# Performance work log

Hardware: AMD Instinct MI355X
Metric: run time of the kernel (lower is better)

Reference implementation:

```python
import jax, jax.numpy as jnp
import numpy as np

B, D_IN, R, D_P, K, D_C, ITERS = 4096, 2048, 7, 128, 25, 16, 3


def _ln(x, g, b, eps=1e-5):
    m = jnp.mean(x, axis=-1, keepdims=True)
    v = jnp.var(x, axis=-1, keepdims=True)
    return (x - m) * jax.lax.rsqrt(v + eps) * g + b


def _squash(x):
    eps = 1e-6
    ns = jnp.sum(x * x, axis=-1, keepdims=True)
    scale = ns / jnp.maximum(1.0 + ns, eps)
    return scale * x / (jnp.sqrt(ns) + eps)


def setup_inputs() -> dict:
    key = jax.random.key(0)
    ks = jax.random.split(key, 8)
    f = lambda k, shp, s=0.02: (jax.random.normal(k, shp) * s).astype(jnp.float32)
    return {
        "z": jax.random.normal(ks[0], (B, D_IN), jnp.float32),
        "W_prim": f(ks[1], (D_IN, R * D_P)),
        "b_prim": jnp.zeros((R * D_P,), jnp.float32),
        "ln_a_g": jnp.ones((D_IN,), jnp.float32),
        "ln_a_b": jnp.zeros((D_IN,), jnp.float32),
        "W_act": f(ks[2], (D_IN, R)),
        "b_act": jnp.zeros((R,), jnp.float32),
        "w_caps": (np.sqrt(K / (D_P * R)).astype(np.float32)
                   * jax.random.normal(ks[3], (R, D_P, K, D_C))).astype(jnp.float32),
        "ln_c_g": jnp.ones((D_C,), jnp.float32),
        "ln_c_b": jnp.zeros((D_C,), jnp.float32),
        "beta_u": f(ks[4], (K,), 1.0),
        "ln_h_g": jnp.ones((R * D_C,), jnp.float32),
        "ln_h_b": jnp.zeros((R * D_C,), jnp.float32),
        "W_h1": f(ks[5], (R * D_C, 4 * R * D_C)),
        "b_h1": jnp.zeros((4 * R * D_C,), jnp.float32),
        "W_h2": f(ks[6], (4 * R * D_C, 1)),
        "b_h2": jnp.zeros((1,), jnp.float32),
    }


def reference(z, W_prim, b_prim, ln_a_g, ln_a_b, W_act, b_act, w_caps,
              ln_c_g, ln_c_b, beta_u, ln_h_g, ln_h_b, W_h1, b_h1, W_h2, b_h2):
    # primary capsules: [B, R, D_P] poses + [B, R] activations
    pose = _squash((z @ W_prim + b_prim).reshape(B, R, D_P))
    act = jnp.clip(jax.nn.sigmoid(_ln(z, ln_a_g, ln_a_b) @ W_act + b_act), 0.0, 1.0)

    # votes: [B, R, K, D_C]
    u = jnp.einsum('brd,rdkh->brkh', pose, w_caps)
    scale = 1.0 / np.sqrt(D_C).astype(np.float32)

    # iterative routing (EM/softmax-agreement style)
    q = jnp.full((B, R, K), 1.0 / K, dtype=z.dtype)
    class_pose = None
    for _ in range(ITERS):
        wts = q * act[:, :, None]                               # [B,R,K]
        class_pose = _ln(jnp.einsum('brk,brkh->bkh', wts, u), ln_c_g, ln_c_b)
        agree = jnp.einsum('bkh,brkh->brk', class_pose, u) * scale
        q = jax.nn.softmax(agree, axis=-1)

    class_act = jax.nn.sigmoid(beta_u[None, :] + jnp.einsum('brk,br->bk', q, act))
    route_class_emb = q[..., None] * u                          # [B,R,K,D_C]

    # concat per-route interaction vectors -> [B, K, R*D_C]
    class_embed = jnp.transpose(route_class_emb, (0, 2, 1, 3)).reshape(B, K, R * D_C)
    h = jax.nn.gelu(_ln(class_embed, ln_h_g, ln_h_b) @ W_h1 + b_h1, approximate=False)
    logits = (h @ W_h2 + b_h2)[..., 0]                          # [B, K]

    return (logits, class_embed, class_pose, class_act, q, pose, act, route_class_emb)
```

## Files before the change

### kernel.cpp

```cpp
#include <hip/hip_runtime.h>
#include <cstddef>

#define BB 4096
#define DIN 2048
#define RR 7
#define DP 128
#define KK 25
#define DC 16
#define NITERS 3
#define RKH (RR*KK*DC)
#define RK  (RR*KK)
#define KH  (KK*DC)
#define HD  (RR*DC)
#define H4  (4*HD)

typedef __attribute__((ext_vector_type(8))) short bf16x8;
typedef __attribute__((ext_vector_type(4))) float f32x4;

__device__ __forceinline__ unsigned pk_bf16(float a, float b) {
    union { float f; unsigned u; } xa, xb;
    xa.f = a; xb.f = b;
    unsigned ua = (xa.u + 0x7FFFu + ((xa.u >> 16) & 1u)) >> 16;
    unsigned ub = (xb.u + 0x7FFFu + ((xb.u >> 16) & 1u)) >> 16;
    return (ua & 0xFFFFu) | (ub << 16);
}

__device__ __forceinline__ float gelu_tanh(float x) {
    float x3 = x * x * x;
    float tt = 0.7978845608f * (x + 0.044715f * x3);
    float e = __expf(2.0f * tt);
    float th = 1.0f - 2.0f / (e + 1.0f);
    return 0.5f * x * (1.0f + th);
}

__global__ __launch_bounds__(256) void transpose_cvt_kernel(
    const float* __restrict__ src, unsigned short* __restrict__ dst, int RS, int CS)
{
    __shared__ float T[64][65];
    int r0 = blockIdx.x * 64, c0 = blockIdx.y * 64;
    size_t bo = (size_t)blockIdx.z * RS * CS;
    src += bo; dst += bo;
    int t = threadIdx.x;
    for (int s = t; s < 64 * 16; s += 256) {
        int row = s >> 4, c4 = s & 15;
        int gr = r0 + row, gc = c0 + c4 * 4;
        float4 v = make_float4(0.f, 0.f, 0.f, 0.f);
        if (gr < RS && gc < CS) v = *(const float4*)(src + (size_t)gr * CS + gc);
        T[row][c4 * 4 + 0] = v.x; T[row][c4 * 4 + 1] = v.y;
        T[row][c4 * 4 + 2] = v.z; T[row][c4 * 4 + 3] = v.w;
    }
    __syncthreads();
    for (int s = t; s < 64 * 16; s += 256) {
        int col = s >> 4, r4 = s & 15;
        int gc = c0 + col, gr = r0 + r4 * 4;
        if (gc < CS && gr + 3 < RS) {
            unsigned lo = pk_bf16(T[r4 * 4 + 0][col], T[r4 * 4 + 1][col]);
            unsigned hi = pk_bf16(T[r4 * 4 + 2][col], T[r4 * 4 + 3][col]);
            *(uint2*)(dst + (size_t)gc * RS + gr) = make_uint2(lo, hi);
        }
    }
}

__global__ __launch_bounds__(256) void act_kernel(
    const float* __restrict__ z, const float* __restrict__ g, const float* __restrict__ bb,
    const float* __restrict__ Wa, const float* __restrict__ ba,
    float* __restrict__ act_out)
{
    int b = blockIdx.x;
    int t = threadIdx.x;
    __shared__ float zs[DIN];
    __shared__ float ws1[4], ws2[4];
    __shared__ float wr[4][RR];
    const float* zr = z + (size_t)b * DIN;
    float s = 0.f, s2 = 0.f;
    for (int i = t; i < DIN; i += 256) {
        float v = zr[i]; zs[i] = v; s += v; s2 += v * v;
    }
    for (int off = 32; off; off >>= 1) { s += __shfl_down(s, off); s2 += __shfl_down(s2, off); }
    int w = t >> 6, lane = t & 63;
    if (lane == 0) { ws1[w] = s; ws2[w] = s2; }
    __syncthreads();
    s  = ws1[0] + ws1[1] + ws1[2] + ws1[3];
    s2 = ws2[0] + ws2[1] + ws2[2] + ws2[3];
    float mean = s * (1.0f / DIN);
    float var  = s2 * (1.0f / DIN) - mean * mean;
    float rstd = rsqrtf(var + 1e-5f);
    float acc[RR];
#pragma unroll
    for (int r = 0; r < RR; ++r) acc[r] = 0.f;
    for (int i = t; i < DIN; i += 256) {
        float y = (zs[i] - mean) * rstd * g[i] + bb[i];
#pragma unroll
        for (int r = 0; r < RR; ++r) acc[r] += y * Wa[i * RR + r];
    }
    for (int off = 32; off; off >>= 1) {
#pragma unroll
        for (int r = 0; r < RR; ++r) acc[r] += __shfl_down(acc[r], off);
    }
    if (lane == 0) {
#pragma unroll
        for (int r = 0; r < RR; ++r) wr[w][r] = acc[r];
    }
    __syncthreads();
    if (t < RR) {
        float v = wr[0][t] + wr[1][t] + wr[2][t] + wr[3][t] + ba[t];
        float sg = 1.0f / (1.0f + expf(-v));
        sg = fminf(fmaxf(sg, 0.0f), 1.0f);
        act_out[(size_t)b * RR + t] = sg;
    }
}

__global__ __launch_bounds__(256) void pose_mfma(
    const float* __restrict__ z, const unsigned short* __restrict__ WpT,
    const float* __restrict__ bp, float* __restrict__ pose_out)
{
    __shared__ __align__(16) unsigned short As[128 * 40];
    __shared__ __align__(16) unsigned short Bs[128 * 40];
    __shared__ float sq[2][128];
    int m0 = blockIdx.x * 128, r = blockIdx.y, t = threadIdx.x;
    int n0 = r * DP;
    int w = t >> 6, l = t & 63;
    int lrow = l & 15, koff = l >> 4;
    int rbase = (w >> 1) * 64, cbase = (w & 1) * 64;
    f32x4 acc[4][4];
#pragma unroll
    for (int i = 0; i < 4; ++i)
#pragma unroll
        for (int j = 0; j < 4; ++j) acc[i][j] = 0.0f;
    for (int kt = 0; kt < DIN; kt += 32) {
#pragma unroll
        for (int q = 0; q < 4; ++q) {
            int s = t + 256 * q;
            int row = s >> 3, k4 = s & 7;
            float4 v = *(const float4*)(z + (size_t)(m0 + row) * DIN + kt + k4 * 4);
            *(uint2*)(As + row * 40 + k4 * 4) = make_uint2(pk_bf16(v.x, v.y), pk_bf16(v.z, v.w));
        }
#pragma unroll
        for (int q = 0; q < 2; ++q) {
            int s = t + 256 * q;
            int col = s >> 2, k8 = s & 3;
            uint4 v = *(const uint4*)(WpT + (size_t)(n0 + col) * DIN + kt + k8 * 8);
            *(uint4*)(Bs + col * 40 + k8 * 8) = v;
        }
        __syncthreads();
        bf16x8 a[4], b[4];
#pragma unroll
        for (int i = 0; i < 4; ++i)
            a[i] = *(const bf16x8*)(As + (rbase + i * 16 + lrow) * 40 + koff * 8);
#pragma unroll
        for (int j = 0; j < 4; ++j)
            b[j] = *(const bf16x8*)(Bs + (cbase + j * 16 + lrow) * 40 + koff * 8);
#pragma unroll
        for (int i = 0; i < 4; ++i)
#pragma unroll
            for (int j = 0; j < 4; ++j)
                acc[i][j] = __builtin_amdgcn_mfma_f32_16x16x32_bf16(a[i], b[j], acc[i][j], 0, 0, 0);
        __syncthreads();
    }
    float bpv[4];
#pragma unroll
    for (int j = 0; j < 4; ++j) bpv[j] = bp[n0 + cbase + j * 16 + lrow];
    float ns_[4][4];
#pragma unroll
    for (int i = 0; i < 4; ++i)
#pragma unroll
        for (int reg = 0; reg < 4; ++reg) {
            float ss = 0.f;
#pragma unroll
            for (int j = 0; j < 4; ++j) {
                float x = acc[i][j][reg] + bpv[j];
                acc[i][j][reg] = x;
                ss += x * x;
            }
            ss += __shfl_xor(ss, 1); ss += __shfl_xor(ss, 2);
            ss += __shfl_xor(ss, 4); ss += __shfl_xor(ss, 8);
            ns_[i][reg] = ss;
        }
    if (lrow == 0) {
#pragma unroll
        for (int i = 0; i < 4; ++i)
#pragma unroll
            for (int reg = 0; reg < 4; ++reg)
                sq[w & 1][rbase + i * 16 + koff * 4 + reg] = ns_[i][reg];
    }
    __syncthreads();
#pragma unroll
    for (int i = 0; i < 4; ++i)
#pragma unroll
        for (int reg = 0; reg < 4; ++reg) {
            int rl = rbase + i * 16 + koff * 4 + reg;
            float ns = sq[0][rl] + sq[1][rl];
            float factor = (ns / fmaxf(1.0f + ns, 1e-6f)) / (sqrtf(ns) + 1e-6f);
            size_t rowbase = ((size_t)(m0 + rl) * RR + r) * DP;
#pragma unroll
            for (int j = 0; j < 4; ++j)
                pose_out[rowbase + cbase + j * 16 + lrow] = acc[i][j][reg] * factor;
        }
}

__global__ __launch_bounds__(256) void votes_mfma(
    const float* __restrict__ pose, const unsigned short* __restrict__ wcT,
    float* __restrict__ u_out)
{
    __shared__ __align__(16) unsigned short As[128 * 152];
    __shared__ __align__(16) unsigned short Bs[80 * 152];
    int m0 = blockIdx.x * 128, r = blockIdx.y, n0 = blockIdx.z * 80;
    int t = threadIdx.x;
    int w = t >> 6, l = t & 63;
    int lrow = l & 15, koff = l >> 4;
    int rbase = w * 32;
#pragma unroll
    for (int q = 0; q < 16; ++q) {
        int s = t + 256 * q;
        int row = s >> 5, k4 = s & 31;
        float4 v = *(const float4*)(pose + ((size_t)(m0 + row) * RR + r) * DP + k4 * 4);
        *(uint2*)(As + row * 152 + k4 * 4) = make_uint2(pk_bf16(v.x, v.y), pk_bf16(v.z, v.w));
    }
    const unsigned short* wr_ = wcT + (size_t)r * KH * DP;
#pragma unroll
    for (int q = 0; q < 5; ++q) {
        int s = t + 256 * q;
        int col = s >> 4, k8 = s & 15;
        uint4 v = *(const uint4*)(wr_ + (size_t)(n0 + col) * DP + k8 * 8);
        *(uint4*)(Bs + col * 152 + k8 * 8) = v;
    }
    __syncthreads();
    f32x4 acc[2][5];
#pragma unroll
    for (int i = 0; i < 2; ++i)
#pragma unroll
        for (int j = 0; j < 5; ++j) acc[i][j] = 0.0f;
#pragma unroll
    for (int ks = 0; ks < 4; ++ks) {
        bf16x8 a[2], b[5];
#pragma unroll
        for (int i = 0; i < 2; ++i)
            a[i] = *(const bf16x8*)(As + (rbase + i * 16 + lrow) * 152 + ks * 32 + koff * 8);
#pragma unroll
        for (int j = 0; j < 5; ++j)
            b[j] = *(const bf16x8*)(Bs + (j * 16 + lrow) * 152 + ks * 32 + koff * 8);
#pragma unroll
        for (int i = 0; i < 2; ++i)
#pragma unroll
            for (int j = 0; j < 5; ++j)
                acc[i][j] = __builtin_amdgcn_mfma_f32_16x16x32_bf16(a[i], b[j], acc[i][j], 0, 0, 0);
    }
#pragma unroll
    for (int i = 0; i < 2; ++i)
#pragma unroll
        for (int reg = 0; reg < 4; ++reg) {
            int row = m0 + rbase + i * 16 + koff * 4 + reg;
            size_t base = ((size_t)row * RR + r) * KH + n0;
#pragma unroll
            for (int j = 0; j < 5; ++j)
                u_out[base + j * 16 + lrow] = acc[i][j][reg];
        }
}

__global__ __launch_bounds__(64) void routing_kernel(
    const float* __restrict__ u_in, const float* __restrict__ act_in,
    const float* __restrict__ lncg, const float* __restrict__ lncb,
    const float* __restrict__ beta_u,
    float* __restrict__ q_out, float* __restrict__ cp_out,
    float* __restrict__ ca_out, float* __restrict__ rce_out,
    float* __restrict__ ce_out)
{
    __shared__ __align__(16) float U[RKH];
    __shared__ float Q[RK];
    __shared__ float CP[KH];
    __shared__ float AG[RK];
    __shared__ float A7[RR];
    int b = blockIdx.x, t = threadIdx.x;
    const float4* u4 = (const float4*)(u_in + (size_t)b * RKH);
    float4* U4 = (float4*)U;
    for (int p = t; p < RKH / 4; p += 64) U4[p] = u4[p];
    if (t < RR) A7[t] = act_in[(size_t)b * RR + t];
    for (int p = t; p < RK; p += 64) Q[p] = 1.0f / KK;
    __syncthreads();
    for (int it = 0; it < NITERS; ++it) {
        for (int p = t; p < KH; p += 64) {
            int k = p / DC;
            float s = 0.f;
#pragma unroll
            for (int r = 0; r < RR; ++r) s += Q[r * KK + k] * A7[r] * U[r * KH + p];
            CP[p] = s;
        }
        __syncthreads();
        if (t < KK) {
            float m = 0.f;
#pragma unroll
            for (int h = 0; h < DC; ++h) m += CP[t * DC + h];
            m *= (1.0f / DC);
            float v = 0.f;
#pragma unroll
            for (int h = 0; h < DC; ++h) { float d = CP[t * DC + h] - m; v += d * d; }
            v *= (1.0f / DC);
            float rstd = rsqrtf(v + 1e-5f);
#pragma unroll
            for (int h = 0; h < DC; ++h)
                CP[t * DC + h] = (CP[t * DC + h] - m) * rstd * lncg[h] + lncb[h];
        }
        __syncthreads();
        for (int p = t; p < RK; p += 64) {
            int r = p / KK, k = p % KK;
            float s = 0.f;
#pragma unroll
            for (int h = 0; h < DC; ++h) s += CP[k * DC + h] * U[r * KH + k * DC + h];
            AG[p] = s * 0.25f;
        }
        __syncthreads();
        if (t < RR) {
            float mx = -1e30f;
            for (int k = 0; k < KK; ++k) mx = fmaxf(mx, AG[t * KK + k]);
            float e[KK], sum = 0.f;
            for (int k = 0; k < KK; ++k) { e[k] = expf(AG[t * KK + k] - mx); sum += e[k]; }
            float inv = 1.0f / sum;
            for (int k = 0; k < KK; ++k) Q[t * KK + k] = e[k] * inv;
        }
        __syncthreads();
    }
    if (t < KK) {
        float s = 0.f;
#pragma unroll
        for (int r = 0; r < RR; ++r) s += Q[r * KK + t] * A7[r];
        ca_out[(size_t)b * KK + t] = 1.0f / (1.0f + expf(-(beta_u[t] + s)));
    }
    for (int p = t; p < RK; p += 64) q_out[(size_t)b * RK + p] = Q[p];
    for (int p = t; p < KH; p += 64) cp_out[(size_t)b * KH + p] = CP[p];
    float4* rce4 = (float4*)(rce_out + (size_t)b * RKH);
    float4* ce4  = (float4*)ce_out;
    for (int p4 = t; p4 < RKH / 4; p4 += 64) {
        int base = p4 * 4;
        int r  = base / KH;
        int k  = (base % KH) / DC;
        int h0 = base % DC;
        float qv = Q[r * KK + k];
        float4 uv = U4[p4];
        float4 rv = make_float4(qv * uv.x, qv * uv.y, qv * uv.z, qv * uv.w);
        rce4[p4] = rv;
        size_t ci = ((size_t)b * RKH + (size_t)k * HD + (size_t)r * DC + h0) >> 2;
        ce4[ci] = rv;
    }
}

__global__ __launch_bounds__(256) void head_mfma(
    const float* __restrict__ ce, const float* __restrict__ g, const float* __restrict__ bb,
    const unsigned short* __restrict__ W1T, const float* __restrict__ b1,
    const float* __restrict__ W2, const float* __restrict__ b2,
    float* __restrict__ logits)
{
    __shared__ __align__(16) unsigned short As[128 * 152];
    __shared__ __align__(16) char pool[64 * 116 * 4];
    __shared__ float gbuf[HD], bbuf[HD];
    float* scr = (float*)pool;
    unsigned short* Bs = (unsigned short*)pool;
    unsigned* As32 = (unsigned*)As;
    unsigned* Bs32 = (unsigned*)Bs;
    int row0 = blockIdx.x * 128;
    int t = threadIdx.x;
    int w = t >> 6, l = t & 63;
    int lrow = l & 15, koff = l >> 4;
    if (t < HD) { gbuf[t] = g[t]; bbuf[t] = bb[t]; }
    for (int p = 0; p < 2; ++p) {
        for (int s = t; s < 64 * 28; s += 256) {
            int row = s / 28, q4 = s % 28;
            float4 v = *(const float4*)(ce + (size_t)(row0 + p * 64 + row) * HD + q4 * 4);
            *(float4*)(scr + row * 116 + q4 * 4) = v;
        }
        __syncthreads();
        {
            int tq = t & 3, row = t >> 2;
            float s1 = 0.f, s2 = 0.f;
            const float* rp = scr + row * 116 + tq * 28;
            for (int q = 0; q < 28; ++q) { float v = rp[q]; s1 += v; s2 += v * v; }
            s1 += __shfl_xor(s1, 1); s2 += __shfl_xor(s2, 1);
            s1 += __shfl_xor(s1, 2); s2 += __shfl_xor(s2, 2);
            float mean = s1 * (1.0f / HD);
            float var  = s2 * (1.0f / HD) - mean * mean;
            float rstd = rsqrtf(var + 1e-5f);
            int grow = p * 64 + row;
            for (int j = 0; j < 14; ++j) {
                int k = tq * 28 + 2 * j;
                float a = (rp[2 * j]     - mean) * rstd * gbuf[k]     + bbuf[k];
                float bv = (rp[2 * j + 1] - mean) * rstd * gbuf[k + 1] + bbuf[k + 1];
                As32[grow * 76 + tq * 14 + j] = pk_bf16(a, bv);
            }
        }
        __syncthreads();
    }
    for (int s = t; s < 128 * 8; s += 256) { int row = s >> 3; As32[row * 76 + 56 + (s & 7)] = 0; }
    for (int s = t; s < 64 * 8;  s += 256) { int col = s >> 3; Bs32[col * 76 + 56 + (s & 7)] = 0; }
    int rbase = w * 32;
    float logitAcc[2][4];
#pragma unroll
    for (int i = 0; i < 2; ++i)
#pragma unroll
        for (int reg = 0; reg < 4; ++reg) logitAcc[i][reg] = 0.f;
    for (int nc = 0; nc < 7; ++nc) {
        __syncthreads();
        for (int s = t; s < 64 * 14; s += 256) {
            int col = s / 14, k4 = s % 14;
            uint4 v = *(const uint4*)(W1T + (size_t)(nc * 64 + col) * HD + k4 * 8);
            *(uint4*)(Bs + col * 152 + k4 * 8) = v;
        }
        __syncthreads();
        f32x4 acc[2][4];
#pragma unroll
        for (int i = 0; i < 2; ++i)
#pragma unroll
            for (int j = 0; j < 4; ++j) acc[i][j] = 0.0f;
#pragma unroll
        for (int ks = 0; ks < 4; ++ks) {
            bf16x8 a[2], b[4];
#pragma unroll
            for (int i = 0; i < 2; ++i)
                a[i] = *(const bf16x8*)(As + (rbase + i * 16 + lrow) * 152 + ks * 32 + koff * 8);
#pragma unroll
            for (int j = 0; j < 4; ++j)
                b[j] = *(const bf16x8*)(Bs + (j * 16 + lrow) * 152 + ks * 32 + koff * 8);
#pragma unroll
            for (int i = 0; i < 2; ++i)
#pragma unroll
                for (int j = 0; j < 4; ++j)
                    acc[i][j] = __builtin_amdgcn_mfma_f32_16x16x32_bf16(a[i], b[j], acc[i][j], 0, 0, 0);
        }
        float b1v[4], w2v[4];
#pragma unroll
        for (int j = 0; j < 4; ++j) {
            b1v[j] = b1[nc * 64 + j * 16 + lrow];
            w2v[j] = W2[nc * 64 + j * 16 + lrow];
        }
#pragma unroll
        for (int i = 0; i < 2; ++i)
#pragma unroll
            for (int reg = 0; reg < 4; ++reg) {
                float sum = 0.f;
#pragma unroll
                for (int j = 0; j < 4; ++j) {
                    float x = acc[i][j][reg] + b1v[j];
                    sum += gelu_tanh(x) * w2v[j];
                }
                logitAcc[i][reg] += sum;
            }
    }
#pragma unroll
    for (int i = 0; i < 2; ++i)
#pragma unroll
        for (int reg = 0; reg < 4; ++reg) {
            float v = logitAcc[i][reg];
            v += __shfl_xor(v, 1); v += __shfl_xor(v, 2);
            v += __shfl_xor(v, 4); v += __shfl_xor(v, 8);
            logitAcc[i][reg] = v;
        }
    if (lrow == 0) {
        float b2v = b2[0];
#pragma unroll
        for (int i = 0; i < 2; ++i)
#pragma unroll
            for (int reg = 0; reg < 4; ++reg)
                logits[row0 + rbase + i * 16 + koff * 4 + reg] = logitAcc[i][reg] + b2v;
    }
}

__global__ __launch_bounds__(256) void pose_kernel(
    const float* __restrict__ z, const float* __restrict__ Wp, const float* __restrict__ bp,
    float* __restrict__ pose_out)
{
    __shared__ __align__(16) float As[64 * 36];
    __shared__ __align__(16) float Bs[32 * 128];
    int m0 = blockIdx.x * 64;
    int r  = blockIdx.y;
    int n0 = r * DP;
    int t  = threadIdx.x;
    int rg = t >> 5;
    int cg = t & 31;
    float acc[8][4] = {};
    for (int kt = 0; kt < DIN; kt += 32) {
#pragma unroll
        for (int q = 0; q < 2; ++q) {
            int s = t * 2 + q;
            int row = s >> 3, k4 = s & 7;
            float4 v = *(const float4*)(z + (size_t)(m0 + row) * DIN + kt + k4 * 4);
            *(float4*)(As + row * 36 + k4 * 4) = v;
        }
#pragma unroll
        for (int q = 0; q < 4; ++q) {
            int s = t + 256 * q;
            int row = s >> 5, c4 = s & 31;
            float4 v = *(const float4*)(Wp + (size_t)(kt + row) * (RR * DP) + n0 + c4 * 4);
            *(float4*)(Bs + row * 128 + c4 * 4) = v;
        }
        __syncthreads();
#pragma unroll
        for (int kk = 0; kk < 32; ++kk) {
            float4 bv = *(const float4*)(Bs + kk * 128 + cg * 4);
#pragma unroll
            for (int j = 0; j < 8; ++j) {
                float a = As[(rg * 8 + j) * 36 + kk];
                acc[j][0] += a * bv.x; acc[j][1] += a * bv.y;
                acc[j][2] += a * bv.z; acc[j][3] += a * bv.w;
            }
        }
        __syncthreads();
    }
    float bi0 = bp[n0 + cg * 4], bi1 = bp[n0 + cg * 4 + 1];
    float bi2 = bp[n0 + cg * 4 + 2], bi3 = bp[n0 + cg * 4 + 3];
#pragma unroll
    for (int j = 0; j < 8; ++j) {
        float x0 = acc[j][0] + bi0, x1 = acc[j][1] + bi1;
        float x2 = acc[j][2] + bi2, x3 = acc[j][3] + bi3;
        float ns = x0 * x0 + x1 * x1 + x2 * x2 + x3 * x3;
        for (int off = 1; off < 32; off <<= 1) ns += __shfl_xor(ns, off);
        float factor = (ns / fmaxf(1.0f + ns, 1e-6f)) / (sqrtf(ns) + 1e-6f);
        int row = m0 + rg * 8 + j;
        float4 o = make_float4(x0 * factor, x1 * factor, x2 * factor, x3 * factor);
        *(float4*)(pose_out + ((size_t)row * RR + r) * DP + cg * 4) = o;
    }
}

__global__ __launch_bounds__(256) void votes_kernel(
    const float* __restrict__ pose, const float* __restrict__ wc,
    float* __restrict__ u_out)
{
    __shared__ float As[64 * 129];
    __shared__ __align__(16) float Bs[64 * 80];
    int m0 = blockIdx.x * 64;
    int r  = blockIdx.y;
    int n0 = blockIdx.z * 80;
    int t  = threadIdx.x;
    const size_t wbase = (size_t)r * DP * KH;
#pragma unroll
    for (int q = 0; q < 8; ++q) {
        int s = t + 256 * q;
        int row = s >> 5, d4 = s & 31;
        float4 v = *(const float4*)(pose + ((size_t)(m0 + row) * RR + r) * DP + d4 * 4);
        As[row * 129 + d4 * 4 + 0] = v.x;
        As[row * 129 + d4 * 4 + 1] = v.y;
        As[row * 129 + d4 * 4 + 2] = v.z;
        As[row * 129 + d4 * 4 + 3] = v.w;
    }
    int m4 = t >> 4, n5 = t & 15;
    float acc[4][5];
#pragma unroll
    for (int i = 0; i < 4; ++i)
#pragma unroll
        for (int j = 0; j < 5; ++j) acc[i][j] = 0.f;
    for (int kt = 0; kt < DP; kt += 64) {
        __syncthreads();
#pragma unroll
        for (int q = 0; q < 5; ++q) {
            int s = t + 256 * q;
            int d = s / 20, c4 = s % 20;
            float4 v = *(const float4*)(wc + wbase + (size_t)(kt + d) * KH + n0 + c4 * 4);
            *(float4*)(Bs + d * 80 + c4 * 4) = v;
        }
        __syncthreads();
#pragma unroll 4
        for (int dd = 0; dd < 64; ++dd) {
            int d = kt + dd;
            float b_[5];
#pragma unroll
            for (int j = 0; j < 5; ++j) b_[j] = Bs[dd * 80 + n5 * 5 + j];
#pragma unroll
            for (int i = 0; i < 4; ++i) {
                float a = As[(m4 * 4 + i) * 129 + d];
#pragma unroll
                for (int j = 0; j < 5; ++j) acc[i][j] += a * b_[j];
            }
        }
    }
#pragma unroll
    for (int i = 0; i < 4; ++i) {
        int row = m0 + m4 * 4 + i;
        size_t base = ((size_t)row * RR + r) * KH + n0 + n5 * 5;
#pragma unroll
        for (int j = 0; j < 5; ++j) u_out[base + j] = acc[i][j];
    }
}

__global__ __launch_bounds__(256) void head_kernel(
    const float* __restrict__ ce, const float* __restrict__ g, const float* __restrict__ bb,
    const float* __restrict__ W1, const float* __restrict__ b1,
    const float* __restrict__ W2, const float* __restrict__ b2,
    float* __restrict__ logits)
{
    __shared__ __align__(16) float Y[64 * HD];
    __shared__ float Wc[HD * 64];
    __shared__ float Lg[64];
    int row0 = blockIdx.x * 64;
    int t = threadIdx.x;
    for (int s = t; s < 64 * HD; s += 256) Y[s] = ce[(size_t)row0 * HD + s];
    __syncthreads();
    if (t < 64) {
        float m = 0.f;
        for (int i = 0; i < HD; ++i) m += Y[t * HD + i];
        m *= (1.0f / HD);
        float v = 0.f;
        for (int i = 0; i < HD; ++i) { float d = Y[t * HD + i] - m; v += d * d; }
        v *= (1.0f / HD);
        float rstd = rsqrtf(v + 1e-5f);
        for (int i = 0; i < HD; ++i) Y[t * HD + i] = (Y[t * HD + i] - m) * rstd * g[i] + bb[i];
    }
    int rg = t >> 4;
    int cg = t & 15;
    float accRow[4] = {0.f, 0.f, 0.f, 0.f};
    for (int c0 = 0; c0 < H4; c0 += 64) {
        __syncthreads();
        for (int s = t; s < HD * 64; s += 256) {
            int i = s >> 6, c = s & 63;
            Wc[i * 64 + c] = W1[(size_t)i * H4 + c0 + c];
        }
        __syncthreads();
        float b1v[4], w2v[4];
#pragma unroll
        for (int c = 0; c < 4; ++c) { b1v[c] = b1[c0 + cg * 4 + c]; w2v[c] = W2[c0 + cg * 4 + c]; }
        float s_[4][4];
#pragma unroll
        for (int rr = 0; rr < 4; ++rr)
#pragma unroll
            for (int c = 0; c < 4; ++c) s_[rr][c] = b1v[c];
        for (int i4 = 0; i4 < HD / 4; ++i4) {
            float4 y4[4];
#pragma unroll
            for (int rr = 0; rr < 4; ++rr)
                y4[rr] = *(const float4*)(Y + (rg * 4 + rr) * HD + i4 * 4);
#pragma unroll
            for (int is = 0; is < 4; ++is) {
                float w_[4];
#pragma unroll
                for (int c = 0; c < 4; ++c) w_[c] = Wc[(i4 * 4 + is) * 64 + cg * 4 + c];
#pragma unroll
                for (int rr = 0; rr < 4; ++rr) {
                    float yv = (is == 0) ? y4[rr].x : (is == 1) ? y4[rr].y : (is == 2) ? y4[rr].z : y4[rr].w;
#pragma unroll
                    for (int c = 0; c < 4; ++c) s_[rr][c] += yv * w_[c];
                }
            }
        }
#pragma unroll
        for (int rr = 0; rr < 4; ++rr) {
#pragma unroll
            for (int c = 0; c < 4; ++c) {
                float x = s_[rr][c];
                float ge = 0.5f * x * (1.0f + erff(x * 0.70710678118654752440f));
                accRow[rr] += ge * w2v[c];
            }
        }
    }
#pragma unroll
    for (int rr = 0; rr < 4; ++rr) {
        float v = accRow[rr];
        v += __shfl_xor(v, 1); v += __shfl_xor(v, 2);
        v += __shfl_xor(v, 4); v += __shfl_xor(v, 8);
        if (cg == 0) Lg[rg * 4 + rr] = v;
    }
    __syncthreads();
    if (t < 64) logits[row0 + t] = Lg[t] + b2[0];
}

extern "C" void kernel_launch(void* const* d_in, const int* in_sizes, int n_in,
                              void* d_out, int out_size, void* d_ws, size_t ws_size,
                              hipStream_t stream) {
    const float* z    = (const float*)d_in[0];
    const float* Wp   = (const float*)d_in[1];
    const float* bp   = (const float*)d_in[2];
    const float* lnag = (const float*)d_in[3];
    const float* lnab = (const float*)d_in[4];
    const float* Wa   = (const float*)d_in[5];
    const float* ba   = (const float*)d_in[6];
    const float* wc   = (const float*)d_in[7];
    const float* lncg = (const float*)d_in[8];
    const float* lncb = (const float*)d_in[9];
    const float* beta = (const float*)d_in[10];
    const float* lnhg = (const float*)d_in[11];
    const float* lnhb = (const float*)d_in[12];
    const float* W1   = (const float*)d_in[13];
    const float* b1   = (const float*)d_in[14];
    const float* W2   = (const float*)d_in[15];
    const float* b2   = (const float*)d_in[16];

    float* out = (float*)d_out;
    float* o_logits = out;
    float* o_ce   = o_logits + (size_t)BB * KK;
    float* o_cp   = o_ce   + (size_t)BB * KK * HD;
    float* o_ca   = o_cp   + (size_t)BB * KK * DC;
    float* o_q    = o_ca   + (size_t)BB * KK;
    float* o_pose = o_q    + (size_t)BB * RK;
    float* o_act  = o_pose + (size_t)BB * RR * DP;
    float* o_rce  = o_act  + (size_t)BB * RR;

    const size_t WPT_ELE = (size_t)(RR * DP) * DIN;
    const size_t W1T_ELE = (size_t)H4 * HD;
    const size_t WCT_ELE = (size_t)RR * KH * DP;
    const size_t WS_NEED = (WPT_ELE + W1T_ELE + WCT_ELE) * sizeof(unsigned short);
    unsigned short* WpT = (unsigned short*)d_ws;
    unsigned short* W1T = WpT + WPT_ELE;
    unsigned short* wcT = W1T + W1T_ELE;

    hipLaunchKernelGGL(act_kernel, dim3(BB), dim3(256), 0, stream,
                       z, lnag, lnab, Wa, ba, o_act);

    if (ws_size >= WS_NEED) {
        hipLaunchKernelGGL(transpose_cvt_kernel, dim3(DIN / 64, (RR * DP) / 64, 1), dim3(256), 0, stream,
                           Wp, WpT, DIN, RR * DP);
        hipLaunchKernelGGL(transpose_cvt_kernel, dim3(2, 7, 1), dim3(256), 0, stream,
                           W1, W1T, HD, H4);
        hipLaunchKernelGGL(transpose_cvt_kernel, dim3(2, 7, RR), dim3(256), 0, stream,
                           wc, wcT, DP, KH);
        hipLaunchKernelGGL(pose_mfma, dim3(BB / 128, RR), dim3(256), 0, stream,
                           z, WpT, bp, o_pose);
        hipLaunchKernelGGL(votes_mfma, dim3(BB / 128, RR, 5), dim3(256), 0, stream,
                           o_pose, wcT, o_rce);
        hipLaunchKernelGGL(routing_kernel, dim3(BB), dim3(64), 0, stream,
                           o_rce, o_act, lncg, lncb, beta, o_q, o_cp, o_ca, o_rce, o_ce);
        hipLaunchKernelGGL(head_mfma, dim3(BB * KK / 128), dim3(256), 0, stream,
                           o_ce, lnhg, lnhb, W1T, b1, W2, b2, o_logits);
    } else {
        hipLaunchKernelGGL(pose_kernel, dim3(BB / 64, RR), dim3(256), 0, stream,
                           z, Wp, bp, o_pose);
        hipLaunchKernelGGL(votes_kernel, dim3(BB / 64, RR, 5), dim3(256), 0, stream,
                           o_pose, wc, o_rce);
        hipLaunchKernelGGL(routing_kernel, dim3(BB), dim3(64), 0, stream,
                           o_rce, o_act, lncg, lncb, beta, o_q, o_cp, o_ca, o_rce, o_ce);
        hipLaunchKernelGGL(head_kernel, dim3(BB * KK / 64), dim3(256), 0, stream,
                           o_ce, lnhg, lnhb, W1, b1, W2, b2, o_logits);
    }
}
```

Measured before the change: 384.0 us.

## Fold LN into act weights, retile pose GEMM, precompute head LN stats

The activation branch now folds the LayerNorm gain and bias into the W_act projection in a one-block prep kernel. Each wave then computes row stats and the dot products in one pass from a shared-memory copy of the folded weights. The pose GEMM moves to 64-row tiles with a 64-wide K step for more blocks and fewer barriers. The routing kernel now emits per-(b,k) LayerNorm mean and rstd, so a new head kernel builds normalized bf16 A fragments directly in registers against a zero-padded W1 transpose. These changes remove redundant reduction passes and shared-memory staging, at the cost of extra workspace and a serialized single-block prep launch.

```diff
diff --git a/kernel.cpp b/kernel.cpp
--- a/kernel.cpp
+++ b/kernel.cpp
@@ -26,20 +26,21 @@
 }
 
 __device__ __forceinline__ float gelu_tanh(float x) {
-    float x3 = x * x * x;
-    float tt = 0.7978845608f * (x + 0.044715f * x3);
+    float x2 = x * x;
+    float tt = x * (0.7978845608f + 0.03567740814f * x2);
     float e = __expf(2.0f * tt);
     float th = 1.0f - 2.0f / (e + 1.0f);
     return 0.5f * x * (1.0f + th);
 }
 
 __global__ __launch_bounds__(256) void transpose_cvt_kernel(
-    const float* __restrict__ src, unsigned short* __restrict__ dst, int RS, int CS)
+    const float* __restrict__ src, unsigned short* __restrict__ dst,
+    int RS, int RSpad, int CS)
 {
     __shared__ float T[64][65];
     int r0 = blockIdx.x * 64, c0 = blockIdx.y * 64;
-    size_t bo = (size_t)blockIdx.z * RS * CS;
-    src += bo; dst += bo;
+    src += (size_t)blockIdx.z * RS * CS;
+    dst += (size_t)blockIdx.z * RSpad * CS;
     int t = threadIdx.x;
     for (int s = t; s < 64 * 16; s += 256) {
         int row = s >> 4, c4 = s & 15;
@@ -53,116 +54,145 @@
     for (int s = t; s < 64 * 16; s += 256) {
         int col = s >> 4, r4 = s & 15;
         int gc = c0 + col, gr = r0 + r4 * 4;
-        if (gc < CS && gr + 3 < RS) {
+        if (gc < CS && gr + 3 < RSpad) {
             unsigned lo = pk_bf16(T[r4 * 4 + 0][col], T[r4 * 4 + 1][col]);
             unsigned hi = pk_bf16(T[r4 * 4 + 2][col], T[r4 * 4 + 3][col]);
-            *(uint2*)(dst + (size_t)gc * RS + gr) = make_uint2(lo, hi);
-        }
-    }
-}
-
-__global__ __launch_bounds__(256) void act_kernel(
-    const float* __restrict__ z, const float* __restrict__ g, const float* __restrict__ bb,
-    const float* __restrict__ Wa, const float* __restrict__ ba,
+            *(uint2*)(dst + (size_t)gc * RSpad + gr) = make_uint2(lo, hi);
+        }
+    }
+}
+
+__global__ __launch_bounds__(256) void prep_act_kernel(
+    const float* __restrict__ g, const float* __restrict__ bvec,
+    const float* __restrict__ Wa, float* __restrict__ Wg, float* __restrict__ GC)
+{
+    __shared__ float red[4];
+    int t = threadIdx.x, w = t >> 6, l = t & 63;
+    float Gp[RR], Cp[RR];
+#pragma unroll
+    for (int r = 0; r < RR; ++r) { Gp[r] = 0.f; Cp[r] = 0.f; }
+    for (int i = t; i < DIN; i += 256) {
+        float gi = g[i], bi = bvec[i];
+#pragma unroll
+        for (int r = 0; r < RR; ++r) {
+            float wv = Wa[i * RR + r];
+            Wg[i * RR + r] = gi * wv;
+            Gp[r] += gi * wv;
+            Cp[r] += bi * wv;
+        }
+    }
+    for (int which = 0; which < 2; ++which) {
+#pragma unroll
+        for (int r = 0; r < RR; ++r) {
+            float v = which ? Cp[r] : Gp[r];
+            for (int off = 32; off; off >>= 1) v += __shfl_down(v, off);
+            if (l == 0) red[w] = v;
+            __syncthreads();
+            if (t == 0) GC[which * RR + r] = red[0] + red[1] + red[2] + red[3];
+            __syncthreads();
+        }
+    }
+}
+
+__global__ __launch_bounds__(256) void act_v2(
+    const float* __restrict__ z, const float* __restrict__ Wg,
+    const float* __restrict__ GC, const float* __restrict__ ba,
     float* __restrict__ act_out)
 {
-    int b = blockIdx.x;
-    int t = threadIdx.x;
-    __shared__ float zs[DIN];
-    __shared__ float ws1[4], ws2[4];
-    __shared__ float wr[4][RR];
-    const float* zr = z + (size_t)b * DIN;
-    float s = 0.f, s2 = 0.f;
-    for (int i = t; i < DIN; i += 256) {
-        float v = zr[i]; zs[i] = v; s += v; s2 += v * v;
-    }
-    for (int off = 32; off; off >>= 1) { s += __shfl_down(s, off); s2 += __shfl_down(s2, off); }
-    int w = t >> 6, lane = t & 63;
-    if (lane == 0) { ws1[w] = s; ws2[w] = s2; }
+    __shared__ float WgS[DIN * RR];
+    __shared__ float GCs[2 * RR];
+    int t = threadIdx.x, w = t >> 6, l = t & 63;
+    for (int s = t; s < DIN * RR; s += 256) WgS[s] = Wg[s];
+    if (t < 2 * RR) GCs[t] = GC[t];
     __syncthreads();
-    s  = ws1[0] + ws1[1] + ws1[2] + ws1[3];
-    s2 = ws2[0] + ws2[1] + ws2[2] + ws2[3];
-    float mean = s * (1.0f / DIN);
-    float var  = s2 * (1.0f / DIN) - mean * mean;
-    float rstd = rsqrtf(var + 1e-5f);
-    float acc[RR];
-#pragma unroll
-    for (int r = 0; r < RR; ++r) acc[r] = 0.f;
-    for (int i = t; i < DIN; i += 256) {
-        float y = (zs[i] - mean) * rstd * g[i] + bb[i];
-#pragma unroll
-        for (int r = 0; r < RR; ++r) acc[r] += y * Wa[i * RR + r];
-    }
-    for (int off = 32; off; off >>= 1) {
-#pragma unroll
-        for (int r = 0; r < RR; ++r) acc[r] += __shfl_down(acc[r], off);
-    }
-    if (lane == 0) {
-#pragma unroll
-        for (int r = 0; r < RR; ++r) wr[w][r] = acc[r];
-    }
-    __syncthreads();
-    if (t < RR) {
-        float v = wr[0][t] + wr[1][t] + wr[2][t] + wr[3][t] + ba[t];
-        float sg = 1.0f / (1.0f + expf(-v));
-        sg = fminf(fmaxf(sg, 0.0f), 1.0f);
-        act_out[(size_t)b * RR + t] = sg;
-    }
-}
-
-__global__ __launch_bounds__(256) void pose_mfma(
+    for (int rr = 0; rr < 2; ++rr) {
+        int row = blockIdx.x * 8 + w * 2 + rr;
+        const float* zr = z + (size_t)row * DIN;
+        float s1 = 0.f, s2 = 0.f, d[RR];
+#pragma unroll
+        for (int r = 0; r < RR; ++r) d[r] = 0.f;
+        for (int q = 0; q < DIN / 64; ++q) {
+            int i = l + 64 * q;
+            float v = zr[i];
+            s1 += v; s2 += v * v;
+#pragma unroll
+            for (int r = 0; r < RR; ++r) d[r] += v * WgS[i * RR + r];
+        }
+        for (int off = 1; off < 64; off <<= 1) {
+            s1 += __shfl_xor(s1, off); s2 += __shfl_xor(s2, off);
+#pragma unroll
+            for (int r = 0; r < RR; ++r) d[r] += __shfl_xor(d[r], off);
+        }
+        float m = s1 * (1.0f / DIN);
+        float var = s2 * (1.0f / DIN) - m * m;
+        float rs = rsqrtf(var + 1e-5f);
+        if (l < RR) {
+            float v = rs * (d[l] - m * GCs[l]) + GCs[RR + l] + ba[l];
+            float sg = 1.0f / (1.0f + expf(-v));
+            act_out[(size_t)row * RR + l] = fminf(fmaxf(sg, 0.0f), 1.0f);
+        }
+    }
+}
+
+__global__ __launch_bounds__(256) void pose64(
     const float* __restrict__ z, const unsigned short* __restrict__ WpT,
     const float* __restrict__ bp, float* __restrict__ pose_out)
 {
-    __shared__ __align__(16) unsigned short As[128 * 40];
-    __shared__ __align__(16) unsigned short Bs[128 * 40];
-    __shared__ float sq[2][128];
-    int m0 = blockIdx.x * 128, r = blockIdx.y, t = threadIdx.x;
-    int n0 = r * DP;
-    int w = t >> 6, l = t & 63;
+    __shared__ __align__(16) unsigned short As[64 * 72];
+    __shared__ __align__(16) unsigned short Bs[128 * 72];
+    __shared__ float sq[2][64];
+    int m0 = blockIdx.x * 64, r = blockIdx.y, n0 = r * DP;
+    int t = threadIdx.x, w = t >> 6, l = t & 63;
     int lrow = l & 15, koff = l >> 4;
-    int rbase = (w >> 1) * 64, cbase = (w & 1) * 64;
-    f32x4 acc[4][4];
-#pragma unroll
-    for (int i = 0; i < 4; ++i)
+    int rhalf = w >> 1, chalf = w & 1;
+    f32x4 acc[2][4];
+#pragma unroll
+    for (int i = 0; i < 2; ++i)
 #pragma unroll
         for (int j = 0; j < 4; ++j) acc[i][j] = 0.0f;
-    for (int kt = 0; kt < DIN; kt += 32) {
+    for (int kt = 0; kt < DIN; kt += 64) {
+#pragma unroll
+        for (int q = 0; q < 2; ++q) {
+            int s = t + 256 * q;
+            int row = s >> 3, e8 = s & 7;
+            const float* p = z + (size_t)(m0 + row) * DIN + kt + e8 * 8;
+            float4 v0 = *(const float4*)p;
+            float4 v1 = *(const float4*)(p + 4);
+            *(uint4*)(As + row * 72 + e8 * 8) =
+                make_uint4(pk_bf16(v0.x, v0.y), pk_bf16(v0.z, v0.w),
+                           pk_bf16(v1.x, v1.y), pk_bf16(v1.z, v1.w));
+        }
 #pragma unroll
         for (int q = 0; q < 4; ++q) {
             int s = t + 256 * q;
-            int row = s >> 3, k4 = s & 7;
-            float4 v = *(const float4*)(z + (size_t)(m0 + row) * DIN + kt + k4 * 4);
-            *(uint2*)(As + row * 40 + k4 * 4) = make_uint2(pk_bf16(v.x, v.y), pk_bf16(v.z, v.w));
-        }
-#pragma unroll
-        for (int q = 0; q < 2; ++q) {
-            int s = t + 256 * q;
-            int col = s >> 2, k8 = s & 3;
-            uint4 v = *(const uint4*)(WpT + (size_t)(n0 + col) * DIN + kt + k8 * 8);
-            *(uint4*)(Bs + col * 40 + k8 * 8) = v;
-        }
-        __syncthreads();
-        bf16x8 a[4], b[4];
-#pragma unroll
-        for (int i = 0; i < 4; ++i)
-            a[i] = *(const bf16x8*)(As + (rbase + i * 16 + lrow) * 40 + koff * 8);
-#pragma unroll
-        for (int j = 0; j < 4; ++j)
-            b[j] = *(const bf16x8*)(Bs + (cbase + j * 16 + lrow) * 40 + koff * 8);
-#pragma unroll
-        for (int i = 0; i < 4; ++i)
+            int col = s >> 3, e8 = s & 7;
+            uint4 v = *(const uint4*)(WpT + (size_t)(n0 + col) * DIN + kt + e8 * 8);
+            *(uint4*)(Bs + col * 72 + e8 * 8) = v;
+        }
+        __syncthreads();
+#pragma unroll
+        for (int ks = 0; ks < 2; ++ks) {
+            bf16x8 a[2], b[4];
+#pragma unroll
+            for (int i = 0; i < 2; ++i)
+                a[i] = *(const bf16x8*)(As + (rhalf * 32 + i * 16 + lrow) * 72 + ks * 32 + koff * 8);
 #pragma unroll
             for (int j = 0; j < 4; ++j)
-                acc[i][j] = __builtin_amdgcn_mfma_f32_16x16x32_bf16(a[i], b[j], acc[i][j], 0, 0, 0);
+                b[j] = *(const bf16x8*)(Bs + (chalf * 64 + j * 16 + lrow) * 72 + ks * 32 + koff * 8);
+#pragma unroll
+            for (int i = 0; i < 2; ++i)
+#pragma unroll
+                for (int j = 0; j < 4; ++j)
+                    acc[i][j] = __builtin_amdgcn_mfma_f32_16x16x32_bf16(a[i], b[j], acc[i][j], 0, 0, 0);
+        }
         __syncthreads();
     }
     float bpv[4];
 #pragma unroll
-    for (int j = 0; j < 4; ++j) bpv[j] = bp[n0 + cbase + j * 16 + lrow];
-    float ns_[4][4];
-#pragma unroll
-    for (int i = 0; i < 4; ++i)
+    for (int j = 0; j < 4; ++j) bpv[j] = bp[n0 + chalf * 64 + j * 16 + lrow];
+    float ns_[2][4];
+#pragma unroll
+    for (int i = 0; i < 2; ++i)
 #pragma unroll
         for (int reg = 0; reg < 4; ++reg) {
             float ss = 0.f;
@@ -178,23 +208,23 @@
         }
     if (lrow == 0) {
 #pragma unroll
-        for (int i = 0; i < 4; ++i)
+        for (int i = 0; i < 2; ++i)
 #pragma unroll
             for (int reg = 0; reg < 4; ++reg)
-                sq[w & 1][rbase + i * 16 + koff * 4 + reg] = ns_[i][reg];
+                sq[chalf][rhalf * 32 + i * 16 + koff * 4 + reg] = ns_[i][reg];
     }
     __syncthreads();
 #pragma unroll
-    for (int i = 0; i < 4; ++i)
+    for (int i = 0; i < 2; ++i)
 #pragma unroll
         for (int reg = 0; reg < 4; ++reg) {
-            int rl = rbase + i * 16 + koff * 4 + reg;
+            int rl = rhalf * 32 + i * 16 + koff * 4 + reg;
             float ns = sq[0][rl] + sq[1][rl];
             float factor = (ns / fmaxf(1.0f + ns, 1e-6f)) / (sqrtf(ns) + 1e-6f);
             size_t rowbase = ((size_t)(m0 + rl) * RR + r) * DP;
 #pragma unroll
             for (int j = 0; j < 4; ++j)
-                pose_out[rowbase + cbase + j * 16 + lrow] = acc[i][j][reg] * factor;
+                pose_out[rowbase + chalf * 64 + j * 16 + lrow] = acc[i][j][reg] * factor;
         }
 }
 
@@ -263,7 +293,7 @@
     const float* __restrict__ beta_u,
     float* __restrict__ q_out, float* __restrict__ cp_out,
     float* __restrict__ ca_out, float* __restrict__ rce_out,
-    float* __restrict__ ce_out)
+    float* __restrict__ ce_out, float2* __restrict__ stats)
 {
     __shared__ __align__(16) float U[RKH];
     __shared__ float Q[RK];
@@ -327,6 +357,25 @@
     }
     for (int p = t; p < RK; p += 64) q_out[(size_t)b * RK + p] = Q[p];
     for (int p = t; p < KH; p += 64) cp_out[(size_t)b * KH + p] = CP[p];
+    if (stats && t < 2 * KK) {
+        int k = t >> 1, s = t & 1;
+        float s1 = 0.f, s2 = 0.f;
+#pragma unroll
+        for (int r = 0; r < RR; ++r) {
+            float qv = Q[r * KK + k];
+#pragma unroll
+            for (int j = 0; j < 8; ++j) {
+                float v = qv * U[r * KH + k * DC + s * 8 + j];
+                s1 += v; s2 += v * v;
+            }
+        }
+        s1 += __shfl_xor(s1, 1); s2 += __shfl_xor(s2, 1);
+        if (s == 0) {
+            float m = s1 * (1.0f / HD);
+            float var = s2 * (1.0f / HD) - m * m;
+            stats[(size_t)b * KK + k] = make_float2(m, rsqrtf(var + 1e-5f));
+        }
+    }
     float4* rce4 = (float4*)(rce_out + (size_t)b * RKH);
     float4* ce4  = (float4*)ce_out;
     for (int p4 = t; p4 < RKH / 4; p4 += 64) {
@@ -340,6 +389,121 @@
         rce4[p4] = rv;
         size_t ci = ((size_t)b * RKH + (size_t)k * HD + (size_t)r * DC + h0) >> 2;
         ce4[ci] = rv;
+    }
+}
+
+__global__ __launch_bounds__(256) void head_v3(
+    const float* __restrict__ ce, const float2* __restrict__ stats,
+    const float* __restrict__ g, const float* __restrict__ bb,
+    const unsigned short* __restrict__ W1Tp, const float* __restrict__ b1,
+    const float* __restrict__ W2, const float* __restrict__ b2,
+    float* __restrict__ logits)
+{
+    __shared__ __align__(16) unsigned short Bs[64 * 136];
+    __shared__ float gbuf[HD], bbuf[HD];
+    int row0 = blockIdx.x * 128;
+    int t = threadIdx.x, w = t >> 6, l = t & 63;
+    int lrow = l & 15, koff = l >> 4;
+    int rbase = w * 32;
+    if (t < HD) { gbuf[t] = g[t]; bbuf[t] = bb[t]; }
+    __syncthreads();
+    bf16x8 afrag[2][4];
+#pragma unroll
+    for (int i = 0; i < 2; ++i) {
+        int row = row0 + rbase + i * 16 + lrow;
+        float2 st = stats[row];
+        float m = st.x, rs = st.y;
+        const float* cr = ce + (size_t)row * HD;
+#pragma unroll
+        for (int ks = 0; ks < 4; ++ks) {
+            int k = ks * 32 + koff * 8;
+            union { bf16x8 v; uint4 u; } fr;
+            if (k < HD) {
+                float4 a0 = *(const float4*)(cr + k);
+                float4 a1 = *(const float4*)(cr + k + 4);
+                float y0 = (a0.x - m) * rs * gbuf[k]     + bbuf[k];
+                float y1 = (a0.y - m) * rs * gbuf[k + 1] + bbuf[k + 1];
+                float y2 = (a0.z - m) * rs * gbuf[k + 2] + bbuf[k + 2];
+                float y3 = (a0.w - m) * rs * gbuf[k + 3] + bbuf[k + 3];
+                float y4 = (a1.x - m) * rs * gbuf[k + 4] + bbuf[k + 4];
+                float y5 = (a1.y - m) * rs * gbuf[k + 5] + bbuf[k + 5];
+                float y6 = (a1.z - m) * rs * gbuf[k + 6] + bbuf[k + 6];
+                float y7 = (a1.w - m) * rs * gbuf[k + 7] + bbuf[k + 7];
+                fr.u = make_uint4(pk_bf16(y0, y1), pk_bf16(y2, y3),
+                                  pk_bf16(y4, y5), pk_bf16(y6, y7));
+            } else {
+                fr.u = make_uint4(0, 0, 0, 0);
+            }
+            afrag[i][ks] = fr.v;
+        }
+    }
+    float logitAcc[2][4];
+#pragma unroll
+    for (int i = 0; i < 2; ++i)
+#pragma unroll
+        for (int reg = 0; reg < 4; ++reg) logitAcc[i][reg] = 0.f;
+    for (int nc = 0; nc < 7; ++nc) {
+        __syncthreads();
+#pragma unroll
+        for (int q = 0; q < 4; ++q) {
+            int s = t + 256 * q;
+            int col = s >> 4, k8 = s & 15;
+            uint4 v = *(const uint4*)(W1Tp + (size_t)(nc * 64 + col) * 128 + k8 * 8);
+            *(uint4*)(Bs + col * 136 + k8 * 8) = v;
+        }
+        __syncthreads();
+        f32x4 acc[2][4];
+#pragma unroll
+        for (int i = 0; i < 2; ++i)
+#pragma unroll
+            for (int j = 0; j < 4; ++j) acc[i][j] = 0.0f;
+#pragma unroll
+        for (int ks = 0; ks < 4; ++ks) {
+            bf16x8 b[4];
+#pragma unroll
+            for (int j = 0; j < 4; ++j)
+                b[j] = *(const bf16x8*)(Bs + (j * 16 + lrow) * 136 + ks * 32 + koff * 8);
+#pragma unroll
+            for (int i = 0; i < 2; ++i)
+#pragma unroll
+                for (int j = 0; j < 4; ++j)
+                    acc[i][j] = __builtin_amdgcn_mfma_f32_16x16x32_bf16(afrag[i][ks], b[j], acc[i][j], 0, 0, 0);
+        }
+        float b1v[4], w2v[4];
+#pragma unroll
+        for (int j = 0; j < 4; ++j) {
+            b1v[j] = b1[nc * 64 + j * 16 + lrow];
+            w2v[j] = W2[nc * 64 + j * 16 + lrow];
+        }
+#pragma unroll
+        for (int i = 0; i < 2; ++i)
+#pragma unroll
+            for (int reg = 0; reg < 4; ++reg) {
+                float sum = 0.f;
+#pragma unroll
+                for (int j = 0; j < 4; ++j) {
+                    float x = acc[i][j][reg] + b1v[j];
+                    sum += gelu_tanh(x) * w2v[j];
+                }
+                logitAcc[i][reg] += sum;
+            }
+    }
+#pragma unroll
+    for (int i = 0; i < 2; ++i)
+#pragma unroll
+        for (int reg = 0; reg < 4; ++reg) {
+            float v = logitAcc[i][reg];
+            v += __shfl_xor(v, 1); v += __shfl_xor(v, 2);
+            v += __shfl_xor(v, 4); v += __shfl_xor(v, 8);
+            logitAcc[i][reg] = v;
+        }
+    if (lrow == 0) {
+        float b2v = b2[0];
+#pragma unroll
+        for (int i = 0; i < 2; ++i)
+#pragma unroll
+            for (int reg = 0; reg < 4; ++reg)
+                logits[row0 + rbase + i * 16 + koff * 4 + reg] = logitAcc[i][reg] + b2v;
     }
 }
 
@@ -459,6 +623,55 @@
 #pragma unroll
             for (int reg = 0; reg < 4; ++reg)
                 logits[row0 + rbase + i * 16 + koff * 4 + reg] = logitAcc[i][reg] + b2v;
+    }
+}
+
+__global__ __launch_bounds__(256) void act_kernel(
+    const float* __restrict__ z, const float* __restrict__ g, const float* __restrict__ bb,
+    const float* __restrict__ Wa, const float* __restrict__ ba,
+    float* __restrict__ act_out)
+{
+    int b = blockIdx.x;
+    int t = threadIdx.x;
+    __shared__ float zs[DIN];
+    __shared__ float ws1[4], ws2[4];
+    __shared__ float wr[4][RR];
+    const float* zr = z + (size_t)b * DIN;
+    float s = 0.f, s2 = 0.f;
+    for (int i = t; i < DIN; i += 256) {
+        float v = zr[i]; zs[i] = v; s += v; s2 += v * v;
+    }
+    for (int off = 32; off; off >>= 1) { s += __shfl_down(s, off); s2 += __shfl_down(s2, off); }
+    int w = t >> 6, lane = t & 63;
+    if (lane == 0) { ws1[w] = s; ws2[w] = s2; }
+    __syncthreads();
+    s  = ws1[0] + ws1[1] + ws1[2] + ws1[3];
+    s2 = ws2[0] + ws2[1] + ws2[2] + ws2[3];
+    float mean = s * (1.0f / DIN);
+    float var  = s2 * (1.0f / DIN) - mean * mean;
+    float rstd = rsqrtf(var + 1e-5f);
+    float acc[RR];
+#pragma unroll
+    for (int r = 0; r < RR; ++r) acc[r] = 0.f;
+    for (int i = t; i < DIN; i += 256) {
+        float y = (zs[i] - mean) * rstd * g[i] + bb[i];
+#pragma unroll
+        for (int r = 0; r < RR; ++r) acc[r] += y * Wa[i * RR + r];
+    }
+    for (int off = 32; off; off >>= 1) {
+#pragma unroll
+        for (int r = 0; r < RR; ++r) acc[r] += __shfl_down(acc[r], off);
+    }
+    if (lane == 0) {
+#pragma unroll
+        for (int r = 0; r < RR; ++r) wr[w][r] = acc[r];
+    }
+    __syncthreads();
+    if (t < RR) {
+        float v = wr[0][t] + wr[1][t] + wr[2][t] + wr[3][t] + ba[t];
+        float sg = 1.0f / (1.0f + expf(-v));
+        sg = fminf(fmaxf(sg, 0.0f), 1.0f);
+        act_out[(size_t)b * RR + t] = sg;
     }
 }
 
@@ -689,39 +902,63 @@
     float* o_act  = o_pose + (size_t)BB * RR * DP;
     float* o_rce  = o_act  + (size_t)BB * RR;
 
-    const size_t WPT_ELE = (size_t)(RR * DP) * DIN;
-    const size_t W1T_ELE = (size_t)H4 * HD;
-    const size_t WCT_ELE = (size_t)RR * KH * DP;
-    const size_t WS_NEED = (WPT_ELE + W1T_ELE + WCT_ELE) * sizeof(unsigned short);
-    unsigned short* WpT = (unsigned short*)d_ws;
-    unsigned short* W1T = WpT + WPT_ELE;
-    unsigned short* wcT = W1T + W1T_ELE;
-
-    hipLaunchKernelGGL(act_kernel, dim3(BB), dim3(256), 0, stream,
-                       z, lnag, lnab, Wa, ba, o_act);
-
-    if (ws_size >= WS_NEED) {
+    const size_t WPT_ELE  = (size_t)(RR * DP) * DIN;
+    const size_t WCT_ELE  = (size_t)RR * KH * DP;
+    const size_t W1TP_ELE = (size_t)H4 * 128;
+    const size_t W1T_ELE  = (size_t)H4 * HD;
+    const size_t STATS_B  = (size_t)BB * KK * sizeof(float2);
+    const size_t WG_B     = (size_t)DIN * RR * sizeof(float);
+    const size_t GC_B     = 64;
+
+    unsigned short* WpT  = (unsigned short*)d_ws;
+    unsigned short* wcT  = WpT + WPT_ELE;
+    unsigned short* W1Tp = wcT + WCT_ELE;
+    float2* stats = (float2*)((char*)(W1Tp + W1TP_ELE));
+    float*  Wg_f  = (float*)((char*)stats + STATS_B);
+    float*  GC_f  = (float*)((char*)Wg_f + WG_B);
+    const size_t WS_FULL = (WPT_ELE + WCT_ELE + W1TP_ELE) * 2 + STATS_B + WG_B + GC_B;
+
+    unsigned short* W1Tm = wcT + WCT_ELE;
+    float* Wg_m = (float*)((char*)(W1Tm + W1T_ELE));
+    float* GC_m = (float*)((char*)Wg_m + WG_B);
+    const size_t WS_MID = (WPT_ELE + WCT_ELE + W1T_ELE) * 2 + WG_B + GC_B;
+
+    if (ws_size >= WS_FULL) {
+        hipLaunchKernelGGL(prep_act_kernel, dim3(1), dim3(256), 0, stream, lnag, lnab, Wa, Wg_f, GC_f);
+        hipLaunchKernelGGL(act_v2, dim3(BB / 8), dim3(256), 0, stream, z, Wg_f, GC_f, ba, o_act);
         hipLaunchKernelGGL(transpose_cvt_kernel, dim3(DIN / 64, (RR * DP) / 64, 1), dim3(256), 0, stream,
-                           Wp, WpT, DIN, RR * DP);
+                           Wp, WpT, DIN, DIN, RR * DP);
         hipLaunchKernelGGL(transpose_cvt_kernel, dim3(2, 7, 1), dim3(256), 0, stream,
-                           W1, W1T, HD, H4);
+                           W1, W1Tp, HD, 128, H4);
         hipLaunchKernelGGL(transpose_cvt_kernel, dim3(2, 7, RR), dim3(256), 0, stream,
-                           wc, wcT, DP, KH);
-        hipLaunchKernelGGL(pose_mfma, dim3(BB / 128, RR), dim3(256), 0, stream,
-                           z, WpT, bp, o_pose);
-        hipLaunchKernelGGL(votes_mfma, dim3(BB / 128, RR, 5), dim3(256), 0, stream,
-                           o_pose, wcT, o_rce);
+                           wc, wcT, DP, DP, KH);
+        hipLaunchKernelGGL(pose64, dim3(BB / 64, RR), dim3(256), 0, stream, z, WpT, bp, o_pose);
+        hipLaunchKernelGGL(votes_mfma, dim3(BB / 128, RR, 5), dim3(256), 0, stream, o_pose, wcT, o_rce);
         hipLaunchKernelGGL(routing_kernel, dim3(BB), dim3(64), 0, stream,
-                           o_rce, o_act, lncg, lncb, beta, o_q, o_cp, o_ca, o_rce, o_ce);
+                           o_rce, o_act, lncg, lncb, beta, o_q, o_cp, o_ca, o_rce, o_ce, stats);
+        hipLaunchKernelGGL(head_v3, dim3(BB * KK / 128), dim3(256), 0, stream,
+                           o_ce, stats, lnhg, lnhb, W1Tp, b1, W2, b2, o_logits);
+    } else if (ws_size >= WS_MID) {
+        hipLaunchKernelGGL(prep_act_kernel, dim3(1), dim3(256), 0, stream, lnag, lnab, Wa, Wg_m, GC_m);
+        hipLaunchKernelGGL(act_v2, dim3(BB / 8), dim3(256), 0, stream, z, Wg_m, GC_m, ba, o_act);
+        hipLaunchKernelGGL(transpose_cvt_kernel, dim3(DIN / 64, (RR * DP) / 64, 1), dim3(256), 0, stream,
+                           Wp, WpT, DIN, DIN, RR * DP);
+        hipLaunchKernelGGL(transpose_cvt_kernel, dim3(2, 7, 1), dim3(256), 0, stream,
+                           W1, W1Tm, HD, HD, H4);
+        hipLaunchKernelGGL(transpose_cvt_kernel, dim3(2, 7, RR), dim3(256), 0, stream,
+                           wc, wcT, DP, DP, KH);
+        hipLaunchKernelGGL(pose64, dim3(BB / 64, RR), dim3(256), 0, stream, z, WpT, bp, o_pose);
+        hipLaunchKernelGGL(votes_mfma, dim3(BB / 128, RR, 5), dim3(256), 0, stream, o_pose, wcT, o_rce);
+        hipLaunchKernelGGL(routing_kernel, dim3(BB), dim3(64), 0, stream,
+                           o_rce, o_act, lncg, lncb, beta, o_q, o_cp, o_ca, o_rce, o_ce, (float2*)nullptr);
         hipLaunchKernelGGL(head_mfma, dim3(BB * KK / 128), dim3(256), 0, stream,
-                           o_ce, lnhg, lnhb, W1T, b1, W2, b2, o_logits);
+                           o_ce, lnhg, lnhb, W1Tm, b1, W2, b2, o_logits);
     } else {
-        hipLaunchKernelGGL(pose_kernel, dim3(BB / 64, RR), dim3(256), 0, stream,
-                           z, Wp, bp, o_pose);
-        hipLaunchKernelGGL(votes_kernel, dim3(BB / 64, RR, 5), dim3(256), 0, stream,
-                           o_pose, wc, o_rce);
+        hipLaunchKernelGGL(act_kernel, dim3(BB), dim3(256), 0, stream, z, lnag, lnab, Wa, ba, o_act);
+        hipLaunchKernelGGL(pose_kernel, dim3(BB / 64, RR), dim3(256), 0, stream, z, Wp, bp, o_pose);
+        hipLaunchKernelGGL(votes_kernel, dim3(BB / 64, RR, 5), dim3(256), 0, stream, o_pose, wc, o_rce);
         hipLaunchKernelGGL(routing_kernel, dim3(BB), dim3(64), 0, stream,
-                           o_rce, o_act, lncg, lncb, beta, o_q, o_cp, o_ca, o_rce, o_ce);
+                           o_rce, o_act, lncg, lncb, beta, o_q, o_cp, o_ca, o_rce, o_ce, (float2*)nullptr);
         hipLaunchKernelGGL(head_kernel, dim3(BB * KK / 64), dim3(256), 0, stream,
                            o_ce, lnhg, lnhb, W1, b1, W2, b2, o_logits);
     }
```

New measurement: 434.5 us. 13.1% more time.
